# Kernel optimization log

Hardware: AMD Instinct MI355X
Metric: run time of the kernel (lower is better)

## Reference

```python
import jax, jax.numpy as jnp
import numpy as np

ARITY = 2
DEPTH = 9          # max_depth: full tree has levels 0..DEPTH
H = 512            # hidden_size
V = 512            # vocab_size
B = 64             # batch
S = 64             # source length


def _preorder_perm(arity, depth):
    # map pre-order position -> flat level-order index
    offs = np.cumsum([0] + [arity ** d for d in range(depth + 1)])
    perm = []
    def rec(d, pos):
        perm.append(int(offs[d] + pos))
        if d < depth:
            for c in range(arity):
                rec(d + 1, pos * arity + c)
    rec(0, 0)
    return np.asarray(perm, dtype=np.int32)

PERM = jnp.asarray(_preorder_perm(ARITY, DEPTH))


def setup_inputs() -> dict:
    key = jax.random.key(0)
    ks = jax.random.split(key, 12)
    s = 0.05
    return {
        "root_hiddens": jax.random.normal(ks[0], (B, H), jnp.float32),
        "ann_emb": jax.random.normal(ks[1], (B, H), jnp.float32),
        "encoder_outputs": jax.random.normal(ks[2], (S, B, H), jnp.float32),
        "source_mask": jnp.ones((B, S), dtype=bool),
        # GRUCell params per child: input_size = 2H (attention concat)
        "w_ih": jax.random.normal(ks[3], (ARITY, 3 * H, 2 * H), jnp.float32) * s,
        "w_hh": jax.random.normal(ks[4], (ARITY, 3 * H, H), jnp.float32) * s,
        "b_ih": jax.random.normal(ks[5], (ARITY, 3 * H), jnp.float32) * s,
        "b_hh": jax.random.normal(ks[6], (ARITY, 3 * H), jnp.float32) * s,
        # hidden2vocab: Linear(H,2H) -> Sigmoid -> Linear(2H,V)
        "W1": jax.random.normal(ks[7], (2 * H, H), jnp.float32) * s,
        "b1": jax.random.normal(ks[8], (2 * H,), jnp.float32) * s,
        "W2": jax.random.normal(ks[9], (V, 2 * H), jnp.float32) * s,
        "b2": jax.random.normal(ks[10], (V,), jnp.float32) * s,
    }


def _gru(x, h, wih, whh, bih, bhh):
    # x: [B,n,2H], h: [B,n,H]; PyTorch GRUCell semantics
    gi = jnp.einsum('bni,gi->bng', x, wih) + bih
    gh = jnp.einsum('bnh,gh->bng', h, whh) + bhh
    i_r, i_z, i_n = jnp.split(gi, 3, axis=-1)
    h_r, h_z, h_n = jnp.split(gh, 3, axis=-1)
    r = jax.nn.sigmoid(i_r + h_r)
    z = jax.nn.sigmoid(i_z + h_z)
    n = jnp.tanh(i_n + r * h_n)
    return (1.0 - z) * n + z * h


def _forward(root_hiddens, ann_emb, encoder_outputs, source_mask,
             w_ih, w_hh, b_ih, b_hh, W1, b1, W2, b2):
    b = root_hiddens.shape[0]
    enc = encoder_outputs.transpose(1, 0, 2)        # [B,S,H]
    h = root_hiddens[:, None, :]                    # [B,1,H]
    prods = []
    for d in range(DEPTH + 1):
        # hidden2vocab at every node of this level
        hid = jax.nn.sigmoid(jnp.einsum('bnh,kh->bnk', h, W1) + b1)
        prods.append(jnp.einsum('bnk,vk->bnv', hid, W2) + b2)
        if d < DEPTH:
            # dot-product attention per node over source positions
            scores = jnp.einsum('bnh,bsh->bns', h, enc)
            scores = jnp.where(source_mask[:, None, :], scores, -1e9)
            a = jax.nn.softmax(scores, axis=-1)
            weighted = jnp.einsum('bns,bsh->bnh', a, enc)
            n = h.shape[1]
            x = jnp.concatenate(
                [jnp.broadcast_to(ann_emb[:, None, :], (b, n, H)), weighted],
                axis=-1)                             # [B,n,2H]
            children = [_gru(x, h, w_ih[c], w_hh[c], b_ih[c], b_hh[c])
                        for c in range(ARITY)]
            h = jnp.stack(children, axis=2).reshape(b, n * ARITY, H)
    out = jnp.concatenate(prods, axis=1)            # [B,N,V] level-order
    out = out[:, PERM, :]                           # pre-order, as torch yields
    return out.transpose(1, 0, 2)                   # [N,B,V] like pad_sequence


def reference(root_hiddens, ann_emb, encoder_outputs, source_mask,
              w_ih, w_hh, b_ih, b_hh, W1, b1, W2, b2):
    return _forward(root_hiddens, ann_emb, encoder_outputs, source_mask,
                    w_ih, w_hh, b_ih, b_hh, W1, b1, W2, b2)
```

## Files before the change

kernel.cpp:

```cpp
#include <hip/hip_runtime.h>


#define BATCH 64
#define HDIM  512

typedef float  floatx4 __attribute__((ext_vector_type(4)));
typedef float  f32x16  __attribute__((ext_vector_type(16)));
typedef short  short8  __attribute__((ext_vector_type(8)));

__device__ __forceinline__ float bf2f(unsigned short u) {
  union { unsigned int i; float f; } v; v.i = ((unsigned int)u) << 16; return v.f;
}
__device__ __forceinline__ unsigned short f2bf(float f) {
  union { float f; unsigned int i; } v; v.f = f;
  unsigned int x = v.i;
  return (unsigned short)((x + 0x7fffu + ((x >> 16) & 1u)) >> 16);
}
__device__ __forceinline__ float sigm(float x) { return 1.f / (1.f + __expf(-x)); }

__device__ __forceinline__ int preorder_idx(int d, int node) {
  int p = 0;
  for (int i = 1; i <= d; ++i) {
    int bit = (node >> (d - i)) & 1;
    p += 1 + bit * ((1 << (10 - i)) - 1);
  }
  return p;
}

__device__ __forceinline__ void stage_f32(unsigned short* ldst, const float* src) {
  float4 v0 = *(const float4*)src;
  float4 v1 = *(const float4*)(src + 4);
  union { unsigned short s[8]; float4 v; } u;
  u.s[0]=f2bf(v0.x); u.s[1]=f2bf(v0.y); u.s[2]=f2bf(v0.z); u.s[3]=f2bf(v0.w);
  u.s[4]=f2bf(v1.x); u.s[5]=f2bf(v1.y); u.s[6]=f2bf(v1.z); u.s[7]=f2bf(v1.w);
  *(float4*)ldst = u.v;
}

__device__ __forceinline__ void stage_split(unsigned short* dh, unsigned short* dl,
                                            const float* src) {
  float4 v0 = *(const float4*)src;
  float4 v1 = *(const float4*)(src + 4);
  float v[8] = {v0.x, v0.y, v0.z, v0.w, v1.x, v1.y, v1.z, v1.w};
  union { unsigned short s[8]; float4 q; } H, L;
  #pragma unroll
  for (int i = 0; i < 8; ++i) {
    unsigned short hb = f2bf(v[i]);
    H.s[i] = hb;
    L.s[i] = f2bf(v[i] - bf2f(hb));
  }
  *(float4*)dh = H.q;
  *(float4*)dl = L.q;
}

__global__ __launch_bounds__(256) void k_root(const float* __restrict__ root,
                                              float* __restrict__ h0,
                                              unsigned short* __restrict__ bh,
                                              unsigned short* __restrict__ bl) {
  int i = blockIdx.x * 256 + threadIdx.x;
  float v = root[i];
  h0[i] = v;
  int row = i >> 9, k = i & 511;
  int mt = row >> 5, r = row & 31, ktg = k >> 4, oct = (k >> 3) & 1, e = k & 7;
  size_t fo = ((size_t)(mt * 32 + ktg) * 64 + oct * 32 + r) * 8 + e;
  unsigned short hb = f2bf(v);
  bh[fo] = hb;
  bl[fo] = f2bf(v - bf2f(hb));
}

__global__ __launch_bounds__(256) void k_prep_wih(const float* __restrict__ wih,
                                                  unsigned short* __restrict__ dh,
                                                  unsigned short* __restrict__ dl) {
  int idx = blockIdx.x * 256 + threadIdx.x;
  int jr  = idx & 31;
  int oct = (idx >> 5) & 1;
  int ktg = (idx >> 6) & 31;
  int jt  = (idx >> 11) & 15;
  int cg  = idx >> 15;
  int c = cg / 3, g = cg % 3;
  int j = jt * 32 + jr, k = ktg * 16 + oct * 8;
  const float* src = wih + ((size_t)c * 1536 + g * 512 + j) * 1024 + 512 + k;
  float v[8];
  *(float4*)&v[0] = *(const float4*)src;
  *(float4*)&v[4] = *(const float4*)(src + 4);
  union { unsigned short s[8]; float4 q; } H, L;
  #pragma unroll
  for (int i = 0; i < 8; ++i) {
    unsigned short hb = f2bf(v[i]); H.s[i] = hb; L.s[i] = f2bf(v[i] - bf2f(hb));
  }
  *(float4*)(dh + (size_t)idx * 8) = H.q;
  *(float4*)(dl + (size_t)idx * 8) = L.q;
}

__global__ __launch_bounds__(256) void k_prep_whh(const float* __restrict__ whh,
                                                  unsigned short* __restrict__ dh,
                                                  unsigned short* __restrict__ dl) {
  int idx = blockIdx.x * 256 + threadIdx.x;
  int jr  = idx & 31;
  int oct = (idx >> 5) & 1;
  int ktg = (idx >> 6) & 31;
  int jt  = (idx >> 11) & 15;
  int cg  = idx >> 15;
  int c = cg / 3, g = cg % 3;
  int j = jt * 32 + jr, k = ktg * 16 + oct * 8;
  const float* src = whh + ((size_t)c * 1536 + g * 512 + j) * 512 + k;
  float v[8];
  *(float4*)&v[0] = *(const float4*)src;
  *(float4*)&v[4] = *(const float4*)(src + 4);
  union { unsigned short s[8]; float4 q; } H, L;
  #pragma unroll
  for (int i = 0; i < 8; ++i) {
    unsigned short hb = f2bf(v[i]); H.s[i] = hb; L.s[i] = f2bf(v[i] - bf2f(hb));
  }
  *(float4*)(dh + (size_t)idx * 8) = H.q;
  *(float4*)(dl + (size_t)idx * 8) = L.q;
}

__global__ __launch_bounds__(256) void k_prep_bf(const float* __restrict__ src,
                                                 unsigned short* __restrict__ db) {
  size_t i = ((size_t)blockIdx.x * 256 + threadIdx.x) * 8;
  stage_f32(db + i, src + i);
}

__global__ __launch_bounds__(256) void k_giann(const float* __restrict__ ann,
                                               const float* __restrict__ wih,
                                               float* __restrict__ giann) {
  __shared__ __align__(16) unsigned short lah[64*40], lal[64*40];
  __shared__ __align__(16) unsigned short lwh[64*40], lwl[64*40];
  int t = threadIdx.x, lane = t & 63, wv = t >> 6;
  int jbase = blockIdx.y * 64, c = blockIdx.z;
  const float* wih_c = wih + (size_t)c * 1536 * 1024;
  floatx4 acc[4];
  #pragma unroll
  for (int i = 0; i < 4; ++i) acc[i] = (floatx4)(0.f);
  int srow = t >> 2, skk = (t & 3) * 8;
  for (int k0 = 0; k0 < 512; k0 += 32) {
    stage_split(lah + srow*40 + skk, lal + srow*40 + skk,
                ann + (size_t)srow * 512 + k0 + skk);
    stage_split(lwh + srow*40 + skk, lwl + srow*40 + skk,
                wih_c + (size_t)(jbase + srow) * 1024 + k0 + skk);
    __syncthreads();
    int arow = wv * 16 + (lane & 15), kq = (lane >> 4) * 8;
    short8 ah = *(const short8*)(lah + arow*40 + kq);
    short8 al = *(const short8*)(lal + arow*40 + kq);
    #pragma unroll
    for (int nt = 0; nt < 4; ++nt) {
      int wo = (nt * 16 + (lane & 15)) * 40 + kq;
      short8 wh = *(const short8*)(lwh + wo);
      short8 wl = *(const short8*)(lwl + wo);
      acc[nt] = __builtin_amdgcn_mfma_f32_16x16x32_bf16(ah, wh, acc[nt], 0, 0, 0);
      acc[nt] = __builtin_amdgcn_mfma_f32_16x16x32_bf16(ah, wl, acc[nt], 0, 0, 0);
      acc[nt] = __builtin_amdgcn_mfma_f32_16x16x32_bf16(al, wh, acc[nt], 0, 0, 0);
    }
    __syncthreads();
  }
  int quad = lane >> 4, cl = lane & 15;
  #pragma unroll
  for (int nt = 0; nt < 4; ++nt) {
    int g = jbase + nt * 16 + cl;
    #pragma unroll
    for (int r = 0; r < 4; ++r) {
      int b = wv * 16 + quad * 4 + r;
      giann[((size_t)c * 64 + b) * 1536 + g] = acc[nt][r];
    }
  }
}

__global__ __launch_bounds__(256) void k_attn(const float* __restrict__ h,
                                              const float* __restrict__ enc,
                                              unsigned short* __restrict__ wgh,
                                              unsigned short* __restrict__ wgl,
                                              int d) {
  int lane = threadIdx.x & 63, wv = threadIdx.x >> 6;
  int m = blockIdx.x * 4 + wv;
  int b = m >> d;
  __shared__ __align__(16) float sh[4][512];
  {
    const float4* src = (const float4*)(h + (size_t)m * HDIM);
    float4* dst = (float4*)sh[wv];
    dst[lane] = src[lane];
    dst[lane + 64] = src[lane + 64];
  }
  __syncthreads();
  const float* hr = sh[wv];
  const float* er = enc + ((size_t)lane * BATCH + b) * HDIM;
  float sc = 0.f;
  for (int k = 0; k < HDIM; k += 8) {
    float4 w0 = *(const float4*)(er + k);
    float4 w1 = *(const float4*)(er + k + 4);
    sc += hr[k+0]*w0.x + hr[k+1]*w0.y + hr[k+2]*w0.z + hr[k+3]*w0.w;
    sc += hr[k+4]*w1.x + hr[k+5]*w1.y + hr[k+6]*w1.z + hr[k+7]*w1.w;
  }
  float mx = sc;
  #pragma unroll
  for (int off = 32; off; off >>= 1) mx = fmaxf(mx, __shfl_xor(mx, off));
  float e = __expf(sc - mx);
  float sum = e;
  #pragma unroll
  for (int off = 32; off; off >>= 1) sum += __shfl_xor(sum, off);
  float a = e / sum;
  float acc[8];
  #pragma unroll
  for (int i = 0; i < 8; ++i) acc[i] = 0.f;
  for (int s = 0; s < 64; ++s) {
    float as = __shfl(a, s);
    const float* ep = enc + ((size_t)s * BATCH + b) * HDIM + lane * 8;
    float4 w0 = *(const float4*)ep;
    float4 w1 = *(const float4*)(ep + 4);
    acc[0] += as * w0.x; acc[1] += as * w0.y; acc[2] += as * w0.z; acc[3] += as * w0.w;
    acc[4] += as * w1.x; acc[5] += as * w1.y; acc[6] += as * w1.z; acc[7] += as * w1.w;
  }
  union { unsigned short s[8]; float4 q; } H, L;
  #pragma unroll
  for (int i = 0; i < 8; ++i) {
    unsigned short hb = f2bf(acc[i]); H.s[i] = hb; L.s[i] = f2bf(acc[i] - bf2f(hb));
  }
  int mt = m >> 5, rr = m & 31;
  size_t fo = ((size_t)(mt * 32 + (lane >> 1)) * 64 + (lane & 1) * 32 + rr) * 8;
  *(float4*)(wgh + fo) = H.q;
  *(float4*)(wgl + fo) = L.q;
}

__global__ __launch_bounds__(256) void k_hid(const float* __restrict__ h,
                                             const unsigned short* __restrict__ W1b,
                                             const float* __restrict__ b1,
                                             unsigned short* __restrict__ hid) {
  __shared__ __align__(16) unsigned short la[64 * 40];
  __shared__ __align__(16) unsigned short lw[64 * 40];
  int t = threadIdx.x, lane = t & 63, wv = t >> 6;
  int mbase = blockIdx.x * 64, jbase = blockIdx.y * 64;
  floatx4 acc[4];
  #pragma unroll
  for (int i = 0; i < 4; ++i) acc[i] = (floatx4)(0.f);
  int srow = t >> 2, skk = (t & 3) * 8;
  for (int k0 = 0; k0 < 512; k0 += 32) {
    stage_f32(la + srow * 40 + skk, h + (size_t)(mbase + srow) * 512 + k0 + skk);
    *(float4*)(lw + srow * 40 + skk) =
        *(const float4*)(W1b + (size_t)(jbase + srow) * 512 + k0 + skk);
    __syncthreads();
    int arow = wv * 16 + (lane & 15);
    int kq = (lane >> 4) * 8;
    short8 af = *(const short8*)(la + arow * 40 + kq);
    #pragma unroll
    for (int nt = 0; nt < 4; ++nt) {
      short8 wf = *(const short8*)(lw + (nt * 16 + (lane & 15)) * 40 + kq);
      acc[nt] = __builtin_amdgcn_mfma_f32_16x16x32_bf16(af, wf, acc[nt], 0, 0, 0);
    }
    __syncthreads();
  }
  int quad = lane >> 4, cl = lane & 15;
  #pragma unroll
  for (int nt = 0; nt < 4; ++nt) {
    int j = jbase + nt * 16 + cl;
    float bias = b1[j];
    #pragma unroll
    for (int r = 0; r < 4; ++r) {
      int m = mbase + wv * 16 + quad * 4 + r;
      hid[(size_t)m * 1024 + j] = f2bf(sigm(acc[nt][r] + bias));
    }
  }
}

__global__ __launch_bounds__(256) void k_out(const unsigned short* __restrict__ hid,
                                             const unsigned short* __restrict__ W2b,
                                             const float* __restrict__ b2,
                                             float* __restrict__ out, int d) {
  __shared__ __align__(16) unsigned short la[64 * 40];
  __shared__ __align__(16) unsigned short lw[64 * 40];
  int t = threadIdx.x, lane = t & 63, wv = t >> 6;
  int mbase = blockIdx.x * 64, jbase = blockIdx.y * 64;
  floatx4 acc[4];
  #pragma unroll
  for (int i = 0; i < 4; ++i) acc[i] = (floatx4)(0.f);
  int srow = t >> 2, skk = (t & 3) * 8;
  for (int k0 = 0; k0 < 1024; k0 += 32) {
    *(float4*)(la + srow * 40 + skk) =
        *(const float4*)(hid + (size_t)(mbase + srow) * 1024 + k0 + skk);
    *(float4*)(lw + srow * 40 + skk) =
        *(const float4*)(W2b + (size_t)(jbase + srow) * 1024 + k0 + skk);
    __syncthreads();
    int arow = wv * 16 + (lane & 15);
    int kq = (lane >> 4) * 8;
    short8 af = *(const short8*)(la + arow * 40 + kq);
    #pragma unroll
    for (int nt = 0; nt < 4; ++nt) {
      short8 wf = *(const short8*)(lw + (nt * 16 + (lane & 15)) * 40 + kq);
      acc[nt] = __builtin_amdgcn_mfma_f32_16x16x32_bf16(af, wf, acc[nt], 0, 0, 0);
    }
    __syncthreads();
  }
  int quad = lane >> 4, cl = lane & 15;
  int nmask = (1 << d) - 1;
  int pv[4], bv[4];
  #pragma unroll
  for (int r = 0; r < 4; ++r) {
    int m = mbase + wv * 16 + quad * 4 + r;
    bv[r] = m >> d;
    pv[r] = preorder_idx(d, m & nmask);
  }
  #pragma unroll
  for (int nt = 0; nt < 4; ++nt) {
    int j = jbase + nt * 16 + cl;
    float bias = b2[j];
    #pragma unroll
    for (int r = 0; r < 4; ++r) {
      out[((size_t)pv[r] * BATCH + bv[r]) * 512 + j] = acc[nt][r] + bias;
    }
  }
}

#define MF32(a, b, c) __builtin_amdgcn_mfma_f32_32x32x16_bf16(a, b, c, 0, 0, 0)

__global__ __launch_bounds__(256, 2) void k_gru(const float* __restrict__ h,
                                             const unsigned short* __restrict__ wgh,
                                             const unsigned short* __restrict__ wgl,
                                             const unsigned short* __restrict__ hbh,
                                             const unsigned short* __restrict__ hbl,
                                             const unsigned short* __restrict__ wihh,
                                             const unsigned short* __restrict__ wihl,
                                             const unsigned short* __restrict__ whhh,
                                             const unsigned short* __restrict__ whhl,
                                             const float* __restrict__ bih,
                                             const float* __restrict__ bhh,
                                             const float* __restrict__ giann,
                                             float* __restrict__ hnext,
                                             unsigned short* __restrict__ nbh,
                                             unsigned short* __restrict__ nbl,
                                             int d, int M, int emit_bf) {
  __shared__ __align__(16) unsigned short trh[128][72], trl[128][72];
  int t = threadIdx.x, lane = t & 63, wv = t >> 6;
  int wm = wv >> 1, wj = wv & 1;
  int c = blockIdx.z;
  int mbase = blockIdx.x * 128, jbase = blockIdx.y * 64;
  int jt_g  = (jbase >> 5) + wj;

  int mtcap = (M >> 5) - 1;
  int mt0 = (mbase >> 5) + wm * 2;
  int mtg0 = mt0 > mtcap ? mtcap : mt0;
  int mtg1 = (mt0 + 1) > mtcap ? mtcap : (mt0 + 1);

  f32x16 a_r[2], a_z[2], a_n[2], a_h[2];
  #pragma unroll
  for (int i = 0; i < 2; ++i) {
    a_r[i] = (f32x16)(0.f); a_z[i] = (f32x16)(0.f);
    a_n[i] = (f32x16)(0.f); a_h[i] = (f32x16)(0.f);
  }

  #pragma unroll
  for (int ph = 0; ph < 2; ++ph) {
    const unsigned short* Ah = ph ? hbh : wgh;
    const unsigned short* Al = ph ? hbl : wgl;
    const unsigned short* Wh = ph ? whhh : wihh;
    const unsigned short* Wl = ph ? whhl : wihl;
    #pragma unroll 2
    for (int k0 = 0; k0 < 512; k0 += 32) {
      int kt = k0 >> 4;
      short8 ah[2][2], al[2][2];
      #pragma unroll
      for (int ktl = 0; ktl < 2; ++ktl) {
        size_t a0 = ((size_t)(mtg0 * 32 + kt + ktl) * 64 + lane) * 8;
        size_t a1 = ((size_t)(mtg1 * 32 + kt + ktl) * 64 + lane) * 8;
        ah[0][ktl] = *(const short8*)(Ah + a0);
        al[0][ktl] = *(const short8*)(Al + a0);
        ah[1][ktl] = *(const short8*)(Ah + a1);
        al[1][ktl] = *(const short8*)(Al + a1);
      }
      short8 w[3][2][2];
      #pragma unroll
      for (int g = 0; g < 3; ++g) {
        size_t base = ((size_t)(((c * 3 + g) * 16 + jt_g) * 32 + kt) * 64
                       + lane) * 8;
        w[g][0][0] = *(const short8*)(Wh + base);
        w[g][0][1] = *(const short8*)(Wl + base);
        w[g][1][0] = *(const short8*)(Wh + base + 512);
        w[g][1][1] = *(const short8*)(Wl + base + 512);
      }
      #pragma unroll
      for (int ktl = 0; ktl < 2; ++ktl) {
        #pragma unroll
        for (int mt = 0; mt < 2; ++mt) {
          short8 AH = ah[mt][ktl], AL = al[mt][ktl];
          a_r[mt] = MF32(AH, w[0][ktl][0], a_r[mt]);
          a_r[mt] = MF32(AH, w[0][ktl][1], a_r[mt]);
          a_r[mt] = MF32(AL, w[0][ktl][0], a_r[mt]);
          a_z[mt] = MF32(AH, w[1][ktl][0], a_z[mt]);
          a_z[mt] = MF32(AH, w[1][ktl][1], a_z[mt]);
          a_z[mt] = MF32(AL, w[1][ktl][0], a_z[mt]);
          if (ph == 0) {
            a_n[mt] = MF32(AH, w[2][ktl][0], a_n[mt]);
            a_n[mt] = MF32(AH, w[2][ktl][1], a_n[mt]);
            a_n[mt] = MF32(AL, w[2][ktl][0], a_n[mt]);
          } else {
            a_h[mt] = MF32(AH, w[2][ktl][0], a_h[mt]);
            a_h[mt] = MF32(AH, w[2][ktl][1], a_h[mt]);
            a_h[mt] = MF32(AL, w[2][ktl][0], a_h[mt]);
          }
        }
      }
    }
  }

  int cl = lane & 31;
  int j = jbase + wj * 32 + cl;
  float br  = bih[c * 1536 + j]        + bhh[c * 1536 + j];
  float bz  = bih[c * 1536 + 512 + j]  + bhh[c * 1536 + 512 + j];
  float bin = bih[c * 1536 + 1024 + j];
  float bhn = bhh[c * 1536 + 1024 + j];
  int rowoff = 4 * (lane >> 5);
  #pragma unroll
  for (int mt = 0; mt < 2; ++mt) {
    int mb0 = mbase + wm * 64 + mt * 32 + rowoff;
    #pragma unroll
    for (int r = 0; r < 16; ++r) {
      int m = mb0 + (r & 3) + 8 * (r >> 2);
      if (m < M) {
        int b = m >> d;
        const float* gp = giann + ((size_t)c * 64 + b) * 1536 + j;
        float rg = sigm(a_r[mt][r] + gp[0] + br);
        float zg = sigm(a_z[mt][r] + gp[512] + bz);
        float ng = tanhf(a_n[mt][r] + gp[1024] + bin + rg * (a_h[mt][r] + bhn));
        float hv = h[(size_t)m * 512 + j];
        float nh = (1.f - zg) * ng + zg * hv;
        hnext[(size_t)(2 * m + c) * 512 + j] = nh;
        if (emit_bf) {
          unsigned short hb = f2bf(nh);
          trh[m - mbase][j - jbase] = hb;
          trl[m - mbase][j - jbase] = f2bf(nh - bf2f(hb));
        }
      }
    }
  }
  if (emit_bf) {
    __syncthreads();
    int a = t >> 7;
    int row = t & 127;
    if (mbase + row < M) {
      const unsigned short* trp = a ? &trl[row][0] : &trh[row][0];
      unsigned short* dst = a ? nbl : nbh;
      int mp = 2 * (mbase + row) + c;
      int mtp = mp >> 5, rp = mp & 31;
      #pragma unroll
      for (int q = 0; q < 8; ++q) {
        int k = jbase + q * 8;
        int ktg = k >> 4, oct = (k >> 3) & 1;
        float4 v = *(const float4*)(trp + q * 8);
        *(float4*)(dst + ((size_t)(mtp * 32 + ktg) * 64 + oct * 32 + rp) * 8) = v;
      }
    }
  }
}

extern "C" void kernel_launch(void* const* d_in, const int* in_sizes, int n_in,
                              void* d_out, int out_size, void* d_ws, size_t ws_size,
                              hipStream_t stream) {
  const float* root = (const float*)d_in[0];
  const float* ann  = (const float*)d_in[1];
  const float* enc  = (const float*)d_in[2];
  const float* wih  = (const float*)d_in[4];
  const float* whh  = (const float*)d_in[5];
  const float* bih  = (const float*)d_in[6];
  const float* bhh  = (const float*)d_in[7];
  const float* W1   = (const float*)d_in[8];
  const float* b1   = (const float*)d_in[9];
  const float* W2   = (const float*)d_in[10];
  const float* b2   = (const float*)d_in[11];
  float* out = (float*)d_out;

  char* ws = (char*)d_ws;
  float* hA = (float*)ws;
  float* hB = (float*)(ws + (size_t)67108864);
  unsigned short* hid  = (unsigned short*)(ws + (size_t)100663296);
  unsigned short* wgh  = (unsigned short*)(ws + (size_t)134217728);
  unsigned short* wgl  = (unsigned short*)(ws + (size_t)150994944);
  unsigned short* hbEh = (unsigned short*)(ws + (size_t)167772160);
  unsigned short* hbEl = (unsigned short*)(ws + (size_t)184549376);
  unsigned short* hbOh = (unsigned short*)(ws + (size_t)201326592);
  unsigned short* hbOl = (unsigned short*)(ws + (size_t)209715200);
  float* giann         = (float*)(ws + (size_t)218103808);
  unsigned short* wihh = (unsigned short*)(ws + (size_t)218890240);
  unsigned short* wihl = (unsigned short*)(ws + (size_t)222035968);
  unsigned short* whhh = (unsigned short*)(ws + (size_t)225181696);
  unsigned short* whhl = (unsigned short*)(ws + (size_t)228327424);
  unsigned short* W1b  = (unsigned short*)(ws + (size_t)231473152);
  unsigned short* W2b  = (unsigned short*)(ws + (size_t)232521728);

  k_root<<<dim3(128), dim3(256), 0, stream>>>(root, hB, hbEh, hbEl);
  k_prep_wih<<<dim3(768), dim3(256), 0, stream>>>(wih, wihh, wihl);
  k_prep_whh<<<dim3(768), dim3(256), 0, stream>>>(whh, whhh, whhl);
  k_prep_bf<<<dim3(256), dim3(256), 0, stream>>>(W1, W1b);
  k_prep_bf<<<dim3(256), dim3(256), 0, stream>>>(W2, W2b);
  k_giann<<<dim3(1, 24, 2), dim3(256), 0, stream>>>(ann, wih, giann);

  float* hcur = hB;
  float* hnxt = hA;
  unsigned short *bhc = hbEh, *blc = hbEl, *bhn = hbOh, *bln = hbOl;
  for (int d = 0; d <= 9; ++d) {
    int n = 1 << d;
    int M = 64 * n;
    k_hid<<<dim3(M / 64, 16), dim3(256), 0, stream>>>(hcur, W1b, b1, hid);
    k_out<<<dim3(M / 64, 8), dim3(256), 0, stream>>>(hid, W2b, b2, out, d);
    if (d < 9) {
      k_attn<<<dim3(M / 4), dim3(256), 0, stream>>>(hcur, enc, wgh, wgl, d);
      k_gru<<<dim3((M + 127) / 128, 8, 2), dim3(256), 0, stream>>>(
          hcur, wgh, wgl, bhc, blc, wihh, wihl, whhh, whhl, bih, bhh, giann,
          hnxt, bhn, bln, d, M, d < 8 ? 1 : 0);
      float* tmp = hcur; hcur = hnxt; hnxt = tmp;
      unsigned short* ts;
      ts = bhc; bhc = bhn; bhn = ts;
      ts = blc; blc = bln; bln = ts;
    }
  }
}
```

Before: 2.443 ms.

## Stage GRU GEMM operands through double-buffered LDS via direct global-to-LDS loads

The GRU kernel's main loop previously had each wave load its A and W fragments straight from global memory into registers, so blocks fetched shared tiles redundantly. Now each k-step's A (hi/lo) and W (hi/lo) fragments are copied into a double-buffered LDS area with global_load_lds, and the next step is prefetched while MFMAs run on the current one. This removes duplicate global traffic across waves and overlaps loads with compute. The cost is a __syncthreads per k-step, a step size of 16 instead of 32, and more LDS per block (about 40KB), which may limit occupancy at the 2-blocks launch bound.

```diff
diff --git a/kernel.cpp b/kernel.cpp
--- a/kernel.cpp
+++ b/kernel.cpp
@@ -25,6 +25,12 @@
     p += 1 + bit * ((1 << (10 - i)) - 1);
   }
   return p;
+}
+
+__device__ __forceinline__ void gload_lds16(const void* g, void* l) {
+  __builtin_amdgcn_global_load_lds(
+      (const __attribute__((address_space(1))) unsigned int*)g,
+      (__attribute__((address_space(3))) unsigned int*)l, 16, 0, 0);
 }
 
 __device__ __forceinline__ void stage_f32(unsigned short* ldst, const float* src) {
@@ -326,17 +332,14 @@
                                              unsigned short* __restrict__ nbh,
                                              unsigned short* __restrict__ nbl,
                                              int d, int M, int emit_bf) {
-  __shared__ __align__(16) unsigned short trh[128][72], trl[128][72];
+  __shared__ __align__(16) unsigned short smem[2][20 * 512];
   int t = threadIdx.x, lane = t & 63, wv = t >> 6;
   int wm = wv >> 1, wj = wv & 1;
   int c = blockIdx.z;
   int mbase = blockIdx.x * 128, jbase = blockIdx.y * 64;
-  int jt_g  = (jbase >> 5) + wj;
-
+  int jt0 = jbase >> 5;
+  int mb32 = mbase >> 5;
   int mtcap = (M >> 5) - 1;
-  int mt0 = (mbase >> 5) + wm * 2;
-  int mtg0 = mt0 > mtcap ? mtcap : mt0;
-  int mtg1 = (mt0 + 1) > mtcap ? mtcap : (mt0 + 1);
 
   f32x16 a_r[2], a_z[2], a_n[2], a_h[2];
   #pragma unroll
@@ -345,60 +348,75 @@
     a_n[i] = (f32x16)(0.f); a_h[i] = (f32x16)(0.f);
   }
 
+  auto stage = [&](int it2, int buf2) {
+    int pht = it2 >> 5, kt = it2 & 31;
+    const unsigned short* Ah = pht ? hbh : wgh;
+    const unsigned short* Al = pht ? hbl : wgl;
+    const unsigned short* Wh = pht ? whhh : wihh;
+    const unsigned short* Wl = pht ? whhl : wihl;
+    #pragma unroll
+    for (int q = 0; q < 5; ++q) {
+      int f = wv * 5 + q;
+      const unsigned short* src;
+      if (f < 8) {
+        int mtl = f >> 1;
+        int mt = mb32 + mtl; if (mt > mtcap) mt = mtcap;
+        const unsigned short* blob = (f & 1) ? Al : Ah;
+        src = blob + ((size_t)(mt * 32 + kt) * 64 + lane) * 8;
+      } else {
+        int u = f - 8;
+        int g = u >> 2, jtl = (u >> 1) & 1;
+        const unsigned short* blob = (u & 1) ? Wl : Wh;
+        src = blob + ((size_t)(((c * 3 + g) * 16 + jt0 + jtl) * 32 + kt) * 64
+                      + lane) * 8;
+      }
+      gload_lds16(src, &smem[buf2][f * 512]);
+    }
+  };
+
+  stage(0, 0);
+  __syncthreads();
   #pragma unroll
   for (int ph = 0; ph < 2; ++ph) {
-    const unsigned short* Ah = ph ? hbh : wgh;
-    const unsigned short* Al = ph ? hbl : wgl;
-    const unsigned short* Wh = ph ? whhh : wihh;
-    const unsigned short* Wl = ph ? whhl : wihl;
-    #pragma unroll 2
-    for (int k0 = 0; k0 < 512; k0 += 32) {
-      int kt = k0 >> 4;
-      short8 ah[2][2], al[2][2];
+    for (int i = 0; i < 32; ++i) {
+      int it = ph * 32 + i;
+      int buf = it & 1;
+      if (it < 63) stage(it + 1, buf ^ 1);
+      const unsigned short* bb = smem[buf];
+      short8 ah[2], al[2];
       #pragma unroll
-      for (int ktl = 0; ktl < 2; ++ktl) {
-        size_t a0 = ((size_t)(mtg0 * 32 + kt + ktl) * 64 + lane) * 8;
-        size_t a1 = ((size_t)(mtg1 * 32 + kt + ktl) * 64 + lane) * 8;
-        ah[0][ktl] = *(const short8*)(Ah + a0);
-        al[0][ktl] = *(const short8*)(Al + a0);
-        ah[1][ktl] = *(const short8*)(Ah + a1);
-        al[1][ktl] = *(const short8*)(Al + a1);
+      for (int mt = 0; mt < 2; ++mt) {
+        int s = (wm * 2 + mt) * 2;
+        ah[mt] = *(const short8*)(bb + s * 512 + lane * 8);
+        al[mt] = *(const short8*)(bb + (s + 1) * 512 + lane * 8);
       }
-      short8 w[3][2][2];
+      short8 w[3][2];
       #pragma unroll
       for (int g = 0; g < 3; ++g) {
-        size_t base = ((size_t)(((c * 3 + g) * 16 + jt_g) * 32 + kt) * 64
-                       + lane) * 8;
-        w[g][0][0] = *(const short8*)(Wh + base);
-        w[g][0][1] = *(const short8*)(Wl + base);
-        w[g][1][0] = *(const short8*)(Wh + base + 512);
-        w[g][1][1] = *(const short8*)(Wl + base + 512);
+        int s = 8 + (g * 2 + wj) * 2;
+        w[g][0] = *(const short8*)(bb + s * 512 + lane * 8);
+        w[g][1] = *(const short8*)(bb + (s + 1) * 512 + lane * 8);
       }
+      f32x16* ax = ph ? a_h : a_n;
       #pragma unroll
-      for (int ktl = 0; ktl < 2; ++ktl) {
-        #pragma unroll
-        for (int mt = 0; mt < 2; ++mt) {
-          short8 AH = ah[mt][ktl], AL = al[mt][ktl];
-          a_r[mt] = MF32(AH, w[0][ktl][0], a_r[mt]);
-          a_r[mt] = MF32(AH, w[0][ktl][1], a_r[mt]);
-          a_r[mt] = MF32(AL, w[0][ktl][0], a_r[mt]);
-          a_z[mt] = MF32(AH, w[1][ktl][0], a_z[mt]);
-          a_z[mt] = MF32(AH, w[1][ktl][1], a_z[mt]);
-          a_z[mt] = MF32(AL, w[1][ktl][0], a_z[mt]);
-          if (ph == 0) {
-            a_n[mt] = MF32(AH, w[2][ktl][0], a_n[mt]);
-            a_n[mt] = MF32(AH, w[2][ktl][1], a_n[mt]);
-            a_n[mt] = MF32(AL, w[2][ktl][0], a_n[mt]);
-          } else {
-            a_h[mt] = MF32(AH, w[2][ktl][0], a_h[mt]);
-            a_h[mt] = MF32(AH, w[2][ktl][1], a_h[mt]);
-            a_h[mt] = MF32(AL, w[2][ktl][0], a_h[mt]);
-          }
-        }
+      for (int mt = 0; mt < 2; ++mt) {
+        short8 AH = ah[mt], AL = al[mt];
+        a_r[mt] = MF32(AH, w[0][0], a_r[mt]);
+        a_r[mt] = MF32(AH, w[0][1], a_r[mt]);
+        a_r[mt] = MF32(AL, w[0][0], a_r[mt]);
+        a_z[mt] = MF32(AH, w[1][0], a_z[mt]);
+        a_z[mt] = MF32(AH, w[1][1], a_z[mt]);
+        a_z[mt] = MF32(AL, w[1][0], a_z[mt]);
+        ax[mt]  = MF32(AH, w[2][0], ax[mt]);
+        ax[mt]  = MF32(AH, w[2][1], ax[mt]);
+        ax[mt]  = MF32(AL, w[2][0], ax[mt]);
       }
-    }
-  }
-
+      __syncthreads();
+    }
+  }
+
+  unsigned short (*trh)[72] = (unsigned short(*)[72])(&smem[0][0]);
+  unsigned short (*trl)[72] = (unsigned short(*)[72])(&smem[0][0] + 128 * 72);
   int cl = lane & 31;
   int j = jbase + wj * 32 + cl;
   float br  = bih[c * 1536 + j]        + bhh[c * 1536 + j];
```

Measured after the change: 2.419 ms. No clear change (-1.0%).
